# Performance work log

Hardware: AMD Instinct MI355X
Metric: run time of the kernel (lower is better)

Reference implementation:

```python
import jax, jax.numpy as jnp
import numpy as np

N = 100000
E = 1600000
IN_C, HID_C, OUT_C = 128, 64, 32


def _add_self_loops(edge_index, n):
    loops = jnp.arange(n, dtype=edge_index.dtype)
    src = jnp.concatenate([edge_index[0], loops])
    dst = jnp.concatenate([edge_index[1], loops])
    return src, dst


def _gcn_norm(src, dst, n):
    # symmetric normalization on A + I with unit edge weights
    deg = jax.ops.segment_sum(jnp.ones_like(dst, dtype=jnp.float32), dst, num_segments=n)
    dinv = jnp.where(deg > 0, jax.lax.rsqrt(deg), 0.0)
    return dinv[src] * dinv[dst]  # [E+N]


def _gcn_conv(x, src, dst, norm, W, b, n):
    h = x @ W                              # [N, out]
    msg = h[src] * norm[:, None]           # [E+N, out]  (dominant gather)
    out = jax.ops.segment_sum(msg, dst, num_segments=n)
    return out + b


def setup_inputs() -> dict:
    key = jax.random.key(0)
    k = jax.random.split(key, 6)
    x = jax.random.normal(k[0], (N, IN_C), dtype=jnp.float32)
    edge_index = jax.random.randint(k[1], (2, E), 0, N, dtype=jnp.int32)
    # Glorot-style init for GCN weights
    W1 = jax.random.normal(k[2], (IN_C, HID_C), dtype=jnp.float32) / np.sqrt(IN_C)
    b1 = jnp.zeros((HID_C,), dtype=jnp.float32)
    W2 = jax.random.normal(k[3], (HID_C, OUT_C), dtype=jnp.float32) / np.sqrt(HID_C)
    b2 = jnp.zeros((OUT_C,), dtype=jnp.float32)
    return {"x": x, "edge_index": edge_index, "W1": W1, "b1": b1, "W2": W2, "b2": b2}


def reference(x, edge_index, W1, b1, W2, b2):
    src, dst = _add_self_loops(edge_index, N)
    norm = _gcn_norm(src, dst, N)
    h = _gcn_conv(x, src, dst, norm, W1, b1, N)
    h = jax.nn.relu(h)
    # dropout p=0.2 is identity in eval mode
    out = _gcn_conv(h, src, dst, norm, W2, b2, N)
    return out
```

## Files before the change

kernel.cpp:

```cpp
#include <hip/hip_runtime.h>
#include <hip/hip_fp16.h>

#define N_NODES 100000
#define E_EDGES 1600000
#define IN_C 128
#define HID_C 64
#define OUT_C 32
#define BNODES 64
#define NBUCK ((N_NODES + BNODES - 1) / BNODES)
#define MAXB 2048
#define NCHUNK 256
#define CHUNK_E (E_EDGES / NCHUNK)

__device__ __forceinline__ int chunk_of_block(int b) { return (b & 7) * (NCHUNK / 8) + (b >> 3); }

__global__ void zero_gcur_kernel(int* __restrict__ gcur) {
    int i = blockIdx.x * 256 + threadIdx.x;
    if (i < NBUCK) gcur[i] = 0;
}

__global__ __launch_bounds__(1024) void bucket_scatter_kernel(const int* __restrict__ src,
                                                              const int* __restrict__ dst,
                                                              int* __restrict__ gcur,
                                                              unsigned* __restrict__ pairs) {
    __shared__ int h[NBUCK];
    for (int i = threadIdx.x; i < NBUCK; i += 1024) h[i] = 0;
    __syncthreads();
    const int chunk = chunk_of_block(blockIdx.x);
    const int base = chunk * CHUNK_E;
    int dc[7];
    int nj = 0;
    for (int j = threadIdx.x; j < CHUNK_E; j += 1024) {
        int d = dst[base + j];
        dc[nj++] = d;
        atomicAdd(&h[d >> 6], 1);
    }
    __syncthreads();
    for (int i = threadIdx.x; i < NBUCK; i += 1024) {
        int c = h[i];
        if (c > 0) h[i] = atomicAdd(&gcur[i], c);
    }
    __syncthreads();
    nj = 0;
    for (int j = threadIdx.x; j < CHUNK_E; j += 1024) {
        int d = dc[nj++];
        int pos = atomicAdd(&h[d >> 6], 1);
        pairs[(unsigned)(d >> 6) * MAXB + (unsigned)pos] =
            ((unsigned)src[base + j] << 6) | (unsigned)(d & 63);
    }
}

__global__ __launch_bounds__(256) void bucket_sort_kernel(const int* __restrict__ gcur,
                                                          unsigned* __restrict__ pairs,
                                                          int* __restrict__ row_beg,
                                                          int* __restrict__ row_end,
                                                          float* __restrict__ dinv) {
    __shared__ unsigned sp[MAXB];
    __shared__ int hcnt[BNODES], scn[BNODES], cur[BNODES];
    const int b = blockIdx.x;
    const int beg = b * MAXB;
    int cnt = gcur[b];
    if (cnt > MAXB) cnt = MAXB;
    if (threadIdx.x < BNODES) hcnt[threadIdx.x] = 0;
    __syncthreads();
    for (int j = threadIdx.x; j < cnt; j += 256) {
        unsigned p = pairs[beg + j];
        sp[j] = p;
        atomicAdd(&hcnt[p & 63], 1);
    }
    __syncthreads();
    if (threadIdx.x < BNODES) scn[threadIdx.x] = hcnt[threadIdx.x];
    __syncthreads();
    for (int off = 1; off < BNODES; off <<= 1) {
        int t = 0;
        if (threadIdx.x < BNODES && threadIdx.x >= off) t = scn[threadIdx.x - off];
        __syncthreads();
        if (threadIdx.x < BNODES) scn[threadIdx.x] += t;
        __syncthreads();
    }
    if (threadIdx.x < BNODES) {
        int ex = scn[threadIdx.x] - hcnt[threadIdx.x];
        cur[threadIdx.x] = ex;
        int node = b * BNODES + threadIdx.x;
        if (node < N_NODES) {
            row_beg[node] = beg + ex;
            row_end[node] = beg + ex + hcnt[threadIdx.x];
            dinv[node] = rsqrtf((float)hcnt[threadIdx.x] + 1.0f);
        }
    }
    __syncthreads();
    for (int j = threadIdx.x; j < cnt; j += 256) {
        unsigned p = sp[j];
        int pos = atomicAdd(&cur[p & 63], 1);
        pairs[beg + pos] = p >> 6;
    }
}

__global__ __launch_bounds__(256) void gemm1_kernel(const float* __restrict__ x,
                                                    const float* __restrict__ W1,
                                                    const float* __restrict__ dinv,
                                                    __half* __restrict__ hs) {
    __shared__ float sW[IN_C * HID_C];
    for (int i = threadIdx.x; i < IN_C * HID_C; i += 256) sW[i] = W1[i];
    __syncthreads();
    const int cg = (threadIdx.x & 7) * 8;
    const int row0 = blockIdx.x * 128 + (threadIdx.x >> 3) * 4;
    float acc[4][8];
#pragma unroll
    for (int r = 0; r < 4; ++r)
#pragma unroll
        for (int c = 0; c < 8; ++c) acc[r][c] = 0.f;

    int rr[4];
#pragma unroll
    for (int r = 0; r < 4; ++r) rr[r] = min(row0 + r, N_NODES - 1);

    const float4* x4 = (const float4*)x;
#pragma unroll 2
    for (int k4 = 0; k4 < IN_C / 4; ++k4) {
        float4 xv[4];
#pragma unroll
        for (int r = 0; r < 4; ++r) xv[r] = x4[(size_t)rr[r] * (IN_C / 4) + k4];
        float xs[4][4];
#pragma unroll
        for (int r = 0; r < 4; ++r) {
            xs[r][0] = xv[r].x; xs[r][1] = xv[r].y; xs[r][2] = xv[r].z; xs[r][3] = xv[r].w;
        }
#pragma unroll
        for (int kk = 0; kk < 4; ++kk) {
            const float4* wp = (const float4*)(sW + (k4 * 4 + kk) * HID_C + cg);
            float4 w0 = wp[0], w1 = wp[1];
            float wv[8] = {w0.x, w0.y, w0.z, w0.w, w1.x, w1.y, w1.z, w1.w};
#pragma unroll
            for (int r = 0; r < 4; ++r)
#pragma unroll
                for (int c = 0; c < 8; ++c)
                    acc[r][c] = fmaf(xs[r][kk], wv[c], acc[r][c]);
        }
    }
#pragma unroll
    for (int r = 0; r < 4; ++r) {
        int row = row0 + r;
        if (row < N_NODES) {
            float dv = dinv[row];
            union { float4 f; __half2 h[4]; } u;
#pragma unroll
            for (int q = 0; q < 4; ++q)
                u.h[q] = __floats2half2_rn(acc[r][2 * q] * dv, acc[r][2 * q + 1] * dv);
            *(float4*)(hs + (size_t)row * HID_C + cg) = u.f;
        }
    }
}

__global__ void agg1_kernel(const int* __restrict__ row_beg, const int* __restrict__ row_end,
                            const int* __restrict__ col,
                            const float2* __restrict__ hsf, const float* __restrict__ dinv,
                            const float* __restrict__ b1, __half* __restrict__ h2h) {
    const int node = blockIdx.x * 16 + (threadIdx.x >> 4);
    const int lane = threadIdx.x & 15;
    if (node >= N_NODES) return;
    const int beg = row_beg[node], end = row_end[node];
    float2 u = hsf[(size_t)node * 16 + lane];
    {
    }
    __half2* uh = (__half2*)&u;
    float2 t0 = __half22float2(uh[0]), t1 = __half22float2(uh[1]);
    float a0 = t0.x, a1 = t0.y, a2 = t1.x, a3 = t1.y;

    int j = beg;
    int idx0 = j + (lane & 7);
    int cv = (idx0 < end) ? col[idx0] : 0;
    while (j + 8 <= end) {
        int jn = j + 8;
        int idxn = jn + (lane & 7);
        int cvn = (idxn < end) ? col[idxn] : 0;
        int s[8];
#pragma unroll
        for (int e = 0; e < 8; ++e) s[e] = __shfl(cv, e, 8);
        float2 v[8];
#pragma unroll
        for (int e = 0; e < 8; ++e) v[e] = hsf[(size_t)s[e] * 16 + lane];
        cv = cvn;
#pragma unroll
        for (int e = 0; e < 8; ++e) {
            __half2* vh = (__half2*)&v[e];
            float2 w0 = __half22float2(vh[0]), w1 = __half22float2(vh[1]);
            a0 += w0.x; a1 += w0.y; a2 += w1.x; a3 += w1.y;
        }
        j = jn;
    }
    const int tail = end - j;
    for (int e = 0; e < tail; ++e) {
        int s = __shfl(cv, e, 8);
        float2 v = hsf[(size_t)s * 16 + lane];
        __half2* vh = (__half2*)&v;
        float2 w0 = __half22float2(vh[0]), w1 = __half22float2(vh[1]);
        a0 += w0.x; a1 += w0.y; a2 += w1.x; a3 += w1.y;
    }
    float dv = dinv[node];
    float4 bb = ((const float4*)b1)[lane];
    union { uint2 w; __half2 h[2]; } pk;
    pk.h[0] = __floats2half2_rn(fmaxf(dv * a0 + bb.x, 0.f), fmaxf(dv * a1 + bb.y, 0.f));
    pk.h[1] = __floats2half2_rn(fmaxf(dv * a2 + bb.z, 0.f), fmaxf(dv * a3 + bb.w, 0.f));
    *(uint2*)(h2h + (size_t)node * HID_C + lane * 4) = pk.w;
}

__global__ __launch_bounds__(256) void gemm2_kernel(const __half* __restrict__ h2h,
                                                    const float* __restrict__ W2,
                                                    const float* __restrict__ dinv,
                                                    __half* __restrict__ gs) {
    __shared__ float sW[HID_C * OUT_C];
    for (int i = threadIdx.x; i < HID_C * OUT_C; i += 256) sW[i] = W2[i];
    __syncthreads();
    const int cg = (threadIdx.x & 3) * 8;
    const int row0 = blockIdx.x * 128 + (threadIdx.x >> 2) * 2;
    float acc[2][8];
#pragma unroll
    for (int r = 0; r < 2; ++r)
#pragma unroll
        for (int c = 0; c < 8; ++c) acc[r][c] = 0.f;

    int rr[2];
#pragma unroll
    for (int r = 0; r < 2; ++r) rr[r] = min(row0 + r, N_NODES - 1);

    const float4* h4 = (const float4*)h2h;
    for (int k8 = 0; k8 < HID_C / 8; ++k8) {
        float xs[2][8];
#pragma unroll
        for (int r = 0; r < 2; ++r) {
            union { float4 f; __half2 h[4]; } u;
            u.f = h4[(size_t)rr[r] * (HID_C / 8) + k8];
#pragma unroll
            for (int q = 0; q < 4; ++q) {
                float2 v = __half22float2(u.h[q]);
                xs[r][2 * q] = v.x; xs[r][2 * q + 1] = v.y;
            }
        }
#pragma unroll
        for (int kk = 0; kk < 8; ++kk) {
            const float4* wp = (const float4*)(sW + (k8 * 8 + kk) * OUT_C + cg);
            float4 w0 = wp[0], w1 = wp[1];
            float wv[8] = {w0.x, w0.y, w0.z, w0.w, w1.x, w1.y, w1.z, w1.w};
#pragma unroll
            for (int r = 0; r < 2; ++r)
#pragma unroll
                for (int c = 0; c < 8; ++c)
                    acc[r][c] = fmaf(xs[r][kk], wv[c], acc[r][c]);
        }
    }
#pragma unroll
    for (int r = 0; r < 2; ++r) {
        int row = row0 + r;
        if (row < N_NODES) {
            float dv = dinv[row];
            union { float4 f; __half2 h[4]; } u;
#pragma unroll
            for (int q = 0; q < 4; ++q)
                u.h[q] = __floats2half2_rn(acc[r][2 * q] * dv, acc[r][2 * q + 1] * dv);
            *(float4*)(gs + (size_t)row * OUT_C + cg) = u.f;
        }
    }
}

__global__ void agg2_kernel(const int* __restrict__ row_beg, const int* __restrict__ row_end,
                            const int* __restrict__ col,
                            const float2* __restrict__ gsf, const float* __restrict__ dinv,
                            const float* __restrict__ b2, float* __restrict__ out) {
    const int node = blockIdx.x * 32 + (threadIdx.x >> 3);
    const int lane = threadIdx.x & 7;
    if (node >= N_NODES) return;
    const int beg = row_beg[node], end = row_end[node];
    float2 u = gsf[(size_t)node * 8 + lane];
    __half2* uh = (__half2*)&u;
    float2 t0 = __half22float2(uh[0]), t1 = __half22float2(uh[1]);
    float a0 = t0.x, a1 = t0.y, a2 = t1.x, a3 = t1.y;

    int j = beg;
    int idx0 = j + lane;
    int cv = (idx0 < end) ? col[idx0] : 0;
    while (j + 8 <= end) {
        int jn = j + 8;
        int idxn = jn + lane;
        int cvn = (idxn < end) ? col[idxn] : 0;
        int s[8];
#pragma unroll
        for (int e = 0; e < 8; ++e) s[e] = __shfl(cv, e, 8);
        float2 v[8];
#pragma unroll
        for (int e = 0; e < 8; ++e) v[e] = gsf[(size_t)s[e] * 8 + lane];
        cv = cvn;
#pragma unroll
        for (int e = 0; e < 8; ++e) {
            __half2* vh = (__half2*)&v[e];
            float2 w0 = __half22float2(vh[0]), w1 = __half22float2(vh[1]);
            a0 += w0.x; a1 += w0.y; a2 += w1.x; a3 += w1.y;
        }
        j = jn;
    }
    const int tail = end - j;
    for (int e = 0; e < tail; ++e) {
        int s = __shfl(cv, e, 8);
        float2 v = gsf[(size_t)s * 8 + lane];
        __half2* vh = (__half2*)&v;
        float2 w0 = __half22float2(vh[0]), w1 = __half22float2(vh[1]);
        a0 += w0.x; a1 += w0.y; a2 += w1.x; a3 += w1.y;
    }
    float dv = dinv[node];
    float4 bb = ((const float4*)b2)[lane];
    float4 o;
    o.x = dv * a0 + bb.x;
    o.y = dv * a1 + bb.y;
    o.z = dv * a2 + bb.z;
    o.w = dv * a3 + bb.w;
    *(float4*)(out + (size_t)node * OUT_C + lane * 4) = o;
}

extern "C" void kernel_launch(void* const* d_in, const int* in_sizes, int n_in,
                              void* d_out, int out_size, void* d_ws, size_t ws_size,
                              hipStream_t stream) {
    const float* x  = (const float*)d_in[0];
    const int*   ei = (const int*)d_in[1];
    const float* W1 = (const float*)d_in[2];
    const float* b1 = (const float*)d_in[3];
    const float* W2 = (const float*)d_in[4];
    const float* b2 = (const float*)d_in[5];
    float* out = (float*)d_out;

    const int* srcv = ei;
    const int* dstv = ei + E_EDGES;

    float* dinv  = (float*)d_ws;
    __half* hs   = (__half*)(dinv + N_NODES);
    __half* h2h  = hs + (size_t)N_NODES * HID_C;
    int* row_beg = (int*)(h2h + (size_t)N_NODES * HID_C);
    int* row_end = row_beg + N_NODES;
    int* gcur    = row_end + N_NODES;
    unsigned* pairs = (unsigned*)(gcur + 1568);
    __half* gs = hs;
    int* col = (int*)pairs;

    zero_gcur_kernel<<<(NBUCK + 255) / 256, 256, 0, stream>>>(gcur);
    bucket_scatter_kernel<<<NCHUNK, 1024, 0, stream>>>(srcv, dstv, gcur, pairs);
    bucket_sort_kernel<<<NBUCK, 256, 0, stream>>>(gcur, pairs, row_beg, row_end, dinv);

    gemm1_kernel<<<(N_NODES + 127) / 128, 256, 0, stream>>>(x, W1, dinv, hs);
    agg1_kernel<<<(N_NODES + 15) / 16, 256, 0, stream>>>(row_beg, row_end, col,
                                                         (const float2*)hs, dinv, b1, h2h);

    gemm2_kernel<<<(N_NODES + 127) / 128, 256, 0, stream>>>(h2h, W2, dinv, gs);
    agg2_kernel<<<(N_NODES + 31) / 32, 256, 0, stream>>>(row_beg, row_end, col,
                                                         (const float2*)gs, dinv, b2, out);
}
```

Measured before the change: 133.2 us.

## Fuse layer-2 GEMM into first aggregation kernel epilogue

The layer-1 aggregation kernel now does the 64x32 W2 multiply itself. Each node's ReLU'd half-precision hidden row is staged in shared memory and the scaled layer-2 features are written directly, so gemm2 and the h2h intermediate buffer are gone. This saves one launch plus a write and reread of a 100000x64 half array. In exchange every aggregation block loads W2 into shared memory and waits at a barrier, and the small per-node matvec may hurt occupancy or lengthen the gather kernel. The grid is now exactly N/16 blocks with no bounds check, so correctness relies on N being divisible by 16.

```diff
diff --git a/kernel.cpp b/kernel.cpp
--- a/kernel.cpp
+++ b/kernel.cpp
@@ -152,17 +152,23 @@
     }
 }
 
-__global__ void agg1_kernel(const int* __restrict__ row_beg, const int* __restrict__ row_end,
-                            const int* __restrict__ col,
-                            const float2* __restrict__ hsf, const float* __restrict__ dinv,
-                            const float* __restrict__ b1, __half* __restrict__ h2h) {
-    const int node = blockIdx.x * 16 + (threadIdx.x >> 4);
+__global__ __launch_bounds__(256) void agg1_kernel(const int* __restrict__ row_beg,
+                                                   const int* __restrict__ row_end,
+                                                   const int* __restrict__ col,
+                                                   const float2* __restrict__ hsf,
+                                                   const float* __restrict__ dinv,
+                                                   const float* __restrict__ b1,
+                                                   const float* __restrict__ W2,
+                                                   __half* __restrict__ gs) {
+    __shared__ float sW[HID_C * OUT_C];
+    __shared__ __half2 sh2[16][HID_C / 2];
+    for (int i = threadIdx.x; i < HID_C * OUT_C; i += 256) sW[i] = W2[i];
+
+    const int nl = threadIdx.x >> 4;
+    const int node = blockIdx.x * 16 + nl;
     const int lane = threadIdx.x & 15;
-    if (node >= N_NODES) return;
     const int beg = row_beg[node], end = row_end[node];
     float2 u = hsf[(size_t)node * 16 + lane];
-    {
-    }
     __half2* uh = (__half2*)&u;
     float2 t0 = __half22float2(uh[0]), t1 = __half22float2(uh[1]);
     float a0 = t0.x, a1 = t0.y, a2 = t1.x, a3 = t1.y;
@@ -197,70 +203,25 @@
         float2 w0 = __half22float2(vh[0]), w1 = __half22float2(vh[1]);
         a0 += w0.x; a1 += w0.y; a2 += w1.x; a3 += w1.y;
     }
-    float dv = dinv[node];
+    const float dv = dinv[node];
     float4 bb = ((const float4*)b1)[lane];
-    union { uint2 w; __half2 h[2]; } pk;
-    pk.h[0] = __floats2half2_rn(fmaxf(dv * a0 + bb.x, 0.f), fmaxf(dv * a1 + bb.y, 0.f));
-    pk.h[1] = __floats2half2_rn(fmaxf(dv * a2 + bb.z, 0.f), fmaxf(dv * a3 + bb.w, 0.f));
-    *(uint2*)(h2h + (size_t)node * HID_C + lane * 4) = pk.w;
-}
-
-__global__ __launch_bounds__(256) void gemm2_kernel(const __half* __restrict__ h2h,
-                                                    const float* __restrict__ W2,
-                                                    const float* __restrict__ dinv,
-                                                    __half* __restrict__ gs) {
-    __shared__ float sW[HID_C * OUT_C];
-    for (int i = threadIdx.x; i < HID_C * OUT_C; i += 256) sW[i] = W2[i];
-    __syncthreads();
-    const int cg = (threadIdx.x & 3) * 8;
-    const int row0 = blockIdx.x * 128 + (threadIdx.x >> 2) * 2;
-    float acc[2][8];
-#pragma unroll
-    for (int r = 0; r < 2; ++r)
-#pragma unroll
-        for (int c = 0; c < 8; ++c) acc[r][c] = 0.f;
-
-    int rr[2];
-#pragma unroll
-    for (int r = 0; r < 2; ++r) rr[r] = min(row0 + r, N_NODES - 1);
-
-    const float4* h4 = (const float4*)h2h;
-    for (int k8 = 0; k8 < HID_C / 8; ++k8) {
-        float xs[2][8];
-#pragma unroll
-        for (int r = 0; r < 2; ++r) {
-            union { float4 f; __half2 h[4]; } u;
-            u.f = h4[(size_t)rr[r] * (HID_C / 8) + k8];
-#pragma unroll
-            for (int q = 0; q < 4; ++q) {
-                float2 v = __half22float2(u.h[q]);
-                xs[r][2 * q] = v.x; xs[r][2 * q + 1] = v.y;
-            }
-        }
-#pragma unroll
-        for (int kk = 0; kk < 8; ++kk) {
-            const float4* wp = (const float4*)(sW + (k8 * 8 + kk) * OUT_C + cg);
-            float4 w0 = wp[0], w1 = wp[1];
-            float wv[8] = {w0.x, w0.y, w0.z, w0.w, w1.x, w1.y, w1.z, w1.w};
-#pragma unroll
-            for (int r = 0; r < 2; ++r)
-#pragma unroll
-                for (int c = 0; c < 8; ++c)
-                    acc[r][c] = fmaf(xs[r][kk], wv[c], acc[r][c]);
-        }
-    }
-#pragma unroll
-    for (int r = 0; r < 2; ++r) {
-        int row = row0 + r;
-        if (row < N_NODES) {
-            float dv = dinv[row];
-            union { float4 f; __half2 h[4]; } u;
-#pragma unroll
-            for (int q = 0; q < 4; ++q)
-                u.h[q] = __floats2half2_rn(acc[r][2 * q] * dv, acc[r][2 * q + 1] * dv);
-            *(float4*)(gs + (size_t)row * OUT_C + cg) = u.f;
-        }
-    }
+    __half2 p0 = __floats2half2_rn(fmaxf(dv * a0 + bb.x, 0.f), fmaxf(dv * a1 + bb.y, 0.f));
+    __half2 p1 = __floats2half2_rn(fmaxf(dv * a2 + bb.z, 0.f), fmaxf(dv * a3 + bb.w, 0.f));
+    sh2[nl][lane * 2] = p0;
+    sh2[nl][lane * 2 + 1] = p1;
+    __syncthreads();
+
+    const int oc = lane * 2;
+    float o0 = 0.f, o1 = 0.f;
+#pragma unroll
+    for (int k2 = 0; k2 < HID_C / 2; ++k2) {
+        float2 hv = __half22float2(sh2[nl][k2]);
+        const float* w0 = sW + (2 * k2) * OUT_C + oc;
+        const float* w1 = sW + (2 * k2 + 1) * OUT_C + oc;
+        o0 = fmaf(hv.x, w0[0], o0); o1 = fmaf(hv.x, w0[1], o1);
+        o0 = fmaf(hv.y, w1[0], o0); o1 = fmaf(hv.y, w1[1], o1);
+    }
+    *(__half2*)(gs + (size_t)node * OUT_C + oc) = __floats2half2_rn(o0 * dv, o1 * dv);
 }
 
 __global__ void agg2_kernel(const int* __restrict__ row_beg, const int* __restrict__ row_end,
@@ -332,12 +293,11 @@
 
     float* dinv  = (float*)d_ws;
     __half* hs   = (__half*)(dinv + N_NODES);
-    __half* h2h  = hs + (size_t)N_NODES * HID_C;
-    int* row_beg = (int*)(h2h + (size_t)N_NODES * HID_C);
+    __half* gs   = hs + (size_t)N_NODES * HID_C;
+    int* row_beg = (int*)(gs + (size_t)N_NODES * OUT_C);
     int* row_end = row_beg + N_NODES;
     int* gcur    = row_end + N_NODES;
     unsigned* pairs = (unsigned*)(gcur + 1568);
-    __half* gs = hs;
     int* col = (int*)pairs;
 
     zero_gcur_kernel<<<(NBUCK + 255) / 256, 256, 0, stream>>>(gcur);
@@ -345,10 +305,10 @@
     bucket_sort_kernel<<<NBUCK, 256, 0, stream>>>(gcur, pairs, row_beg, row_end, dinv);
 
     gemm1_kernel<<<(N_NODES + 127) / 128, 256, 0, stream>>>(x, W1, dinv, hs);
-    agg1_kernel<<<(N_NODES + 15) / 16, 256, 0, stream>>>(row_beg, row_end, col,
-                                                         (const float2*)hs, dinv, b1, h2h);
-
-    gemm2_kernel<<<(N_NODES + 127) / 128, 256, 0, stream>>>(h2h, W2, dinv, gs);
+
+    agg1_kernel<<<N_NODES / 16, 256, 0, stream>>>(row_beg, row_end, col,
+                                                  (const float2*)hs, dinv, b1, W2, gs);
+
     agg2_kernel<<<(N_NODES + 31) / 32, 256, 0, stream>>>(row_beg, row_end, col,
                                                          (const float2*)gs, dinv, b2, out);
 }
```

Measured after the change: 128.7 us. 1.03x faster.

## Split hidden features into two 32-channel slices for aggregation locality

Applied to the files above, without the earlier changes.

The first GEMM now writes its fp16 output as two planar slices of 32 channels, each with a 64-byte row. The first aggregation runs one block per slice, so each slice's gathered working set is half as large and fits better in L2/MALL. The second GEMM reads the sliced layout, and gs gets its own buffer instead of aliasing hs. The node-bound checks are dropped because N is divisible by 32, and the column index list is now read twice, once per slice.

```diff
diff --git a/kernel.cpp b/kernel.cpp
--- a/kernel.cpp
+++ b/kernel.cpp
@@ -138,6 +138,8 @@
                     acc[r][c] = fmaf(xs[r][kk], wv[c], acc[r][c]);
         }
     }
+    const int sl = cg >> 5;
+    const int off = cg & 31;
 #pragma unroll
     for (int r = 0; r < 4; ++r) {
         int row = row0 + r;
@@ -147,39 +149,43 @@
 #pragma unroll
             for (int q = 0; q < 4; ++q)
                 u.h[q] = __floats2half2_rn(acc[r][2 * q] * dv, acc[r][2 * q + 1] * dv);
-            *(float4*)(hs + (size_t)row * HID_C + cg) = u.f;
-        }
-    }
-}
-
-__global__ void agg1_kernel(const int* __restrict__ row_beg, const int* __restrict__ row_end,
-                            const int* __restrict__ col,
-                            const float2* __restrict__ hsf, const float* __restrict__ dinv,
-                            const float* __restrict__ b1, __half* __restrict__ h2h) {
-    const int node = blockIdx.x * 16 + (threadIdx.x >> 4);
-    const int lane = threadIdx.x & 15;
-    if (node >= N_NODES) return;
+            *(float4*)(hs + ((size_t)sl * N_NODES + row) * 32 + off) = u.f;
+        }
+    }
+}
+
+__global__ __launch_bounds__(256) void agg1_kernel(const int* __restrict__ row_beg,
+                                                   const int* __restrict__ row_end,
+                                                   const int* __restrict__ col,
+                                                   const __half* __restrict__ hs,
+                                                   const float* __restrict__ dinv,
+                                                   const float* __restrict__ b1,
+                                                   __half* __restrict__ h2h) {
+    const int slice = blockIdx.x & 1;
+    const int ng = blockIdx.x >> 1;
+    const int node = ng * 32 + (threadIdx.x >> 3);
+    const int lane = threadIdx.x & 7;
+    const float2* hsf = (const float2*)(hs + (size_t)slice * N_NODES * 32);
     const int beg = row_beg[node], end = row_end[node];
-    float2 u = hsf[(size_t)node * 16 + lane];
-    {
-    }
+
+    float2 u = hsf[(size_t)node * 8 + lane];
     __half2* uh = (__half2*)&u;
     float2 t0 = __half22float2(uh[0]), t1 = __half22float2(uh[1]);
     float a0 = t0.x, a1 = t0.y, a2 = t1.x, a3 = t1.y;
 
     int j = beg;
-    int idx0 = j + (lane & 7);
+    int idx0 = j + lane;
     int cv = (idx0 < end) ? col[idx0] : 0;
     while (j + 8 <= end) {
         int jn = j + 8;
-        int idxn = jn + (lane & 7);
+        int idxn = jn + lane;
         int cvn = (idxn < end) ? col[idxn] : 0;
         int s[8];
 #pragma unroll
         for (int e = 0; e < 8; ++e) s[e] = __shfl(cv, e, 8);
         float2 v[8];
 #pragma unroll
-        for (int e = 0; e < 8; ++e) v[e] = hsf[(size_t)s[e] * 16 + lane];
+        for (int e = 0; e < 8; ++e) v[e] = hsf[(size_t)s[e] * 8 + lane];
         cv = cvn;
 #pragma unroll
         for (int e = 0; e < 8; ++e) {
@@ -192,17 +198,17 @@
     const int tail = end - j;
     for (int e = 0; e < tail; ++e) {
         int s = __shfl(cv, e, 8);
-        float2 v = hsf[(size_t)s * 16 + lane];
+        float2 v = hsf[(size_t)s * 8 + lane];
         __half2* vh = (__half2*)&v;
         float2 w0 = __half22float2(vh[0]), w1 = __half22float2(vh[1]);
         a0 += w0.x; a1 += w0.y; a2 += w1.x; a3 += w1.y;
     }
-    float dv = dinv[node];
-    float4 bb = ((const float4*)b1)[lane];
+    const float dv = dinv[node];
+    float4 bb = ((const float4*)b1)[slice * 8 + lane];
     union { uint2 w; __half2 h[2]; } pk;
     pk.h[0] = __floats2half2_rn(fmaxf(dv * a0 + bb.x, 0.f), fmaxf(dv * a1 + bb.y, 0.f));
     pk.h[1] = __floats2half2_rn(fmaxf(dv * a2 + bb.z, 0.f), fmaxf(dv * a3 + bb.w, 0.f));
-    *(uint2*)(h2h + (size_t)node * HID_C + lane * 4) = pk.w;
+    *(uint2*)(h2h + ((size_t)slice * N_NODES + node) * 32 + lane * 4) = pk.w;
 }
 
 __global__ __launch_bounds__(256) void gemm2_kernel(const __half* __restrict__ h2h,
@@ -230,7 +236,7 @@
 #pragma unroll
         for (int r = 0; r < 2; ++r) {
             union { float4 f; __half2 h[4]; } u;
-            u.f = h4[(size_t)rr[r] * (HID_C / 8) + k8];
+            u.f = h4[((size_t)(k8 >> 2) * N_NODES + rr[r]) * 4 + (k8 & 3)];
 #pragma unroll
             for (int q = 0; q < 4; ++q) {
                 float2 v = __half22float2(u.h[q]);
@@ -269,7 +275,6 @@
                             const float* __restrict__ b2, float* __restrict__ out) {
     const int node = blockIdx.x * 32 + (threadIdx.x >> 3);
     const int lane = threadIdx.x & 7;
-    if (node >= N_NODES) return;
     const int beg = row_beg[node], end = row_end[node];
     float2 u = gsf[(size_t)node * 8 + lane];
     __half2* uh = (__half2*)&u;
@@ -333,11 +338,11 @@
     float* dinv  = (float*)d_ws;
     __half* hs   = (__half*)(dinv + N_NODES);
     __half* h2h  = hs + (size_t)N_NODES * HID_C;
-    int* row_beg = (int*)(h2h + (size_t)N_NODES * HID_C);
+    __half* gs   = h2h + (size_t)N_NODES * HID_C;
+    int* row_beg = (int*)(gs + (size_t)N_NODES * OUT_C);
     int* row_end = row_beg + N_NODES;
     int* gcur    = row_end + N_NODES;
     unsigned* pairs = (unsigned*)(gcur + 1568);
-    __half* gs = hs;
     int* col = (int*)pairs;
 
     zero_gcur_kernel<<<(NBUCK + 255) / 256, 256, 0, stream>>>(gcur);
@@ -345,10 +350,12 @@
     bucket_sort_kernel<<<NBUCK, 256, 0, stream>>>(gcur, pairs, row_beg, row_end, dinv);
 
     gemm1_kernel<<<(N_NODES + 127) / 128, 256, 0, stream>>>(x, W1, dinv, hs);
-    agg1_kernel<<<(N_NODES + 15) / 16, 256, 0, stream>>>(row_beg, row_end, col,
-                                                         (const float2*)hs, dinv, b1, h2h);
+
+    agg1_kernel<<<2 * (N_NODES / 32), 256, 0, stream>>>(row_beg, row_end, col, hs,
+                                                        dinv, b1, h2h);
 
     gemm2_kernel<<<(N_NODES + 127) / 128, 256, 0, stream>>>(h2h, W2, dinv, gs);
-    agg2_kernel<<<(N_NODES + 31) / 32, 256, 0, stream>>>(row_beg, row_end, col,
-                                                         (const float2*)gs, dinv, b2, out);
-}
+
+    agg2_kernel<<<N_NODES / 32, 256, 0, stream>>>(row_beg, row_end, col,
+                                                  (const float2*)gs, dinv, b2, out);
+}
```

Result: slower. 136.9 us (+2.7%).
